# Performance work log

Hardware: AMD Instinct MI355X
Metric: run time of the kernel (lower is better)

Reference implementation:

```python
import jax, jax.numpy as jnp
import numpy as np

B, M, D, H = 2, 2048, 1024, 16
DH = D // H            # 64 head dim
FF = 2624              # GeGLU intermediate size
EPS = 1e-5
ROPE_BASE = 10000.0


def _layernorm(x, g, b):
    mu = jnp.mean(x, axis=-1, keepdims=True)
    var = jnp.mean(jnp.square(x - mu), axis=-1, keepdims=True)
    return (x - mu) * jax.lax.rsqrt(var + EPS) * g + b


def _rope_cos_sin(m, dh):
    # HF-style: inv_freq over even dims; only first dh/2 entries are used by apply_rope
    inv_freq = 1.0 / (ROPE_BASE ** (jnp.arange(0, dh, 2, dtype=jnp.float32) / dh))  # [dh/2]
    ang = jnp.arange(m, dtype=jnp.float32)[:, None] * inv_freq[None, :]             # [M, dh/2]
    return jnp.cos(ang), jnp.sin(ang)


def _apply_rope(x, c, s):
    # x: [B,H,M,dh]; c,s: [M,dh/2] broadcast over B,H. Half-split (non-interleaved) rotation.
    x1, x2 = jnp.split(x, 2, axis=-1)
    return jnp.concatenate([x1 * c - x2 * s, x1 * s + x2 * c], axis=-1)


def setup_inputs() -> dict:
    key = jax.random.key(0)
    ks = jax.random.split(key, 6)
    w = lambda k, shape: (jax.random.normal(k, shape, jnp.float32) * 0.02)
    return {
        "hidden_states": jax.random.normal(ks[0], (B, M, D), jnp.float32),
        "attention_mask": jnp.ones((B, M), jnp.int32),
        "ln1_g": jnp.ones((D,), jnp.float32),
        "ln1_b": jnp.zeros((D,), jnp.float32),
        "Wqkv_w": w(ks[1], (3 * D, D)),
        "Wqkv_b": jnp.zeros((3 * D,), jnp.float32),
        "Wo_w": w(ks[2], (D, D)),
        "ln2_g": jnp.ones((D,), jnp.float32),
        "ln2_b": jnp.zeros((D,), jnp.float32),
        "Wi_w": w(ks[3], (2 * FF, D)),
        "Wmlp_o_w": w(ks[4], (D, FF)),
    }


def reference(hidden_states, attention_mask, ln1_g, ln1_b, Wqkv_w, Wqkv_b, Wo_w,
              ln2_g, ln2_b, Wi_w, Wmlp_o_w):
    x = hidden_states                                    # [B,M,D]
    xn = _layernorm(x, ln1_g, ln1_b)
    qkv = xn @ Wqkv_w.T + Wqkv_b                         # [B,M,3D]
    qkv = qkv.reshape(B, M, 3, H, DH).transpose(0, 3, 1, 2, 4)  # [B,H,M,3,dh]
    q, k, v = qkv[..., 0, :], qkv[..., 1, :], qkv[..., 2, :]    # each [B,H,M,dh]

    c, s = _rope_cos_sin(M, DH)                          # [M, dh/2]
    q = _apply_rope(q, c, s)
    k = _apply_rope(k, c, s)

    scale = 1.0 / np.sqrt(DH)
    scores = jnp.einsum("bhmd,bhnd->bhmn", q, k) * scale  # [B,H,M,M]
    keep = (attention_mask > 0)[:, None, None, :]         # [B,1,1,M] padding mask on keys
    scores = jnp.where(keep, scores, -jnp.inf)
    p = jax.nn.softmax(scores, axis=-1)
    o = jnp.einsum("bhmn,bhnd->bhmd", p, v)               # [B,H,M,dh]

    attn_out = o.transpose(0, 2, 1, 3).reshape(B, M, D)
    x = x + attn_out @ Wo_w.T

    # ModernBERT GeGLU MLP: input, gate = Wi(x).chunk(2); Wo(gelu(input) * gate)
    xn2 = _layernorm(x, ln2_g, ln2_b)
    hg = xn2 @ Wi_w.T                                     # [B,M,2*FF]
    h_in, h_gate = jnp.split(hg, 2, axis=-1)
    x = x + (jax.nn.gelu(h_in) * h_gate) @ Wmlp_o_w.T
    return x
```

## Files before the change

### kernel.cpp

```cpp
#include <hip/hip_runtime.h>
#include <cstdint>
#include <cstddef>

using u16 = unsigned short;
using u32 = uint32_t;

typedef __attribute__((ext_vector_type(8))) short short8;
typedef __attribute__((ext_vector_type(4))) float floatx4;

#define DEVFN static __device__ __forceinline__

#define QSCALE 0.18033688011112042f

DEVFN u16 f2bf(float f) {
  u32 u = __float_as_uint(f);
  return (u16)((u + 0x7fffu + ((u >> 16) & 1u)) >> 16);
}

DEVFN float b2f(u16 u) { return __uint_as_float(((u32)u) << 16); }

DEVFN void async_load16(const void* g, const void* lds) {
  __builtin_amdgcn_global_load_lds(
      (const __attribute__((address_space(1))) u32*)(uintptr_t)g,
      (__attribute__((address_space(3))) u32*)(u32)(uintptr_t)lds,
      16, 0, 0);
}

DEVFN void cvt4(const float* __restrict__ src, u16* __restrict__ dst, int i) {
  const float4 v = ((const float4*)src)[i];
  ushort4 o;
  o.x = f2bf(v.x); o.y = f2bf(v.y); o.z = f2bf(v.z); o.w = f2bf(v.w);
  ((ushort4*)dst)[i] = o;
}

__global__ __launch_bounds__(256)
void prep_k(const float* __restrict__ Wqkv, const float* __restrict__ Wo,
            const float* __restrict__ Wi, const float* __restrict__ Wmlp,
            const float* __restrict__ hidden, const float* __restrict__ ln1g,
            const float* __restrict__ ln1b,
            u16* __restrict__ wqkv_bf, u16* __restrict__ wo_bf,
            u16* __restrict__ wi_bf, u16* __restrict__ wmlp_bf,
            float* __restrict__ ct, float* __restrict__ st, u16* __restrict__ xn) {
  const int bid = blockIdx.x;
  const int tid = threadIdx.x;
  __shared__ float red[8];
  if (bid < 256) {
    const int i = bid * 256 + tid;
    const int m = i >> 5, f = i & 31;
    const float inv = exp2f((float)f * -0.41524101186092025f);
    const float ang = (float)m * inv;
    ct[i] = cosf(ang);
    st[i] = sinf(ang);
  } else if (bid < 3328) {
    cvt4(Wqkv, wqkv_bf, (bid - 256) * 256 + tid);
  } else if (bid < 4352) {
    cvt4(Wo, wo_bf, (bid - 3328) * 256 + tid);
  } else if (bid < 9600) {
    const int i = (bid - 4352) * 256 + tid;
    const int i4 = i * 4;
    const int p = i4 >> 10, kc = i4 & 1023;
    const int g = p >> 5, c = p & 31;
    const int srow = (c < 16) ? (g * 16 + c) : (2624 + g * 16 + (c - 16));
    const float4 v = *(const float4*)(Wi + (size_t)srow * 1024 + kc);
    ushort4 o;
    o.x = f2bf(v.x); o.y = f2bf(v.y); o.z = f2bf(v.z); o.w = f2bf(v.w);
    ((ushort4*)wi_bf)[i] = o;
  } else if (bid < 12224) {
    cvt4(Wmlp, wmlp_bf, (bid - 9600) * 256 + tid);
  } else {
    const int row = bid - 12224;
    const float4 v = ((const float4*)(hidden + (size_t)row * 1024))[tid];
    float s = v.x + v.y + v.z + v.w;
    float ss = v.x * v.x + v.y * v.y + v.z * v.z + v.w * v.w;
#pragma unroll
    for (int d = 32; d > 0; d >>= 1) {
      s += __shfl_xor(s, d);
      ss += __shfl_xor(ss, d);
    }
    const int wave = tid >> 6;
    if ((tid & 63) == 0) { red[wave] = s; red[4 + wave] = ss; }
    __syncthreads();
    s = red[0] + red[1] + red[2] + red[3];
    ss = red[4] + red[5] + red[6] + red[7];
    const float mu = s * (1.f / 1024.f);
    const float var = ss * (1.f / 1024.f) - mu * mu;
    const float rr = rsqrtf(var + 1e-5f);
    const float4 gv = ((const float4*)ln1g)[tid];
    const float4 bv = ((const float4*)ln1b)[tid];
    u16* orow = xn + (size_t)row * 1024 + tid * 4;
    orow[0] = f2bf((v.x - mu) * rr * gv.x + bv.x);
    orow[1] = f2bf((v.y - mu) * rr * gv.y + bv.y);
    orow[2] = f2bf((v.z - mu) * rr * gv.z + bv.z);
    orow[3] = f2bf((v.w - mu) * rr * gv.w + bv.w);
  }
}

__global__ __launch_bounds__(256)
void red_ln_k(const float* __restrict__ resid, const u16* __restrict__ p0,
              const u16* __restrict__ p1, const u16* __restrict__ p2,
              const float* __restrict__ g, const float* __restrict__ bb,
              float* __restrict__ outx, u16* __restrict__ outn) {
  const int row = blockIdx.x;
  const int tid = threadIdx.x;
  const size_t base = (size_t)row * 1024;
  const float4 h = ((const float4*)(resid + base))[tid];
  const ushort4 a = ((const ushort4*)(p0 + base))[tid];
  const ushort4 c = ((const ushort4*)(p1 + base))[tid];
  const ushort4 d = ((const ushort4*)(p2 + base))[tid];
  float4 v;
  v.x = h.x + b2f(a.x) + b2f(c.x) + b2f(d.x);
  v.y = h.y + b2f(a.y) + b2f(c.y) + b2f(d.y);
  v.z = h.z + b2f(a.z) + b2f(c.z) + b2f(d.z);
  v.w = h.w + b2f(a.w) + b2f(c.w) + b2f(d.w);
  float s = v.x + v.y + v.z + v.w;
  float ss = v.x * v.x + v.y * v.y + v.z * v.z + v.w * v.w;
#pragma unroll
  for (int dd = 32; dd > 0; dd >>= 1) {
    s += __shfl_xor(s, dd);
    ss += __shfl_xor(ss, dd);
  }
  __shared__ float red[8];
  const int wave = tid >> 6;
  if ((tid & 63) == 0) { red[wave] = s; red[4 + wave] = ss; }
  __syncthreads();
  s = red[0] + red[1] + red[2] + red[3];
  ss = red[4] + red[5] + red[6] + red[7];
  const float mu = s * (1.f / 1024.f);
  const float var = ss * (1.f / 1024.f) - mu * mu;
  const float rr = rsqrtf(var + 1e-5f);
  ((float4*)(outx + base))[tid] = v;
  const float4 gv = ((const float4*)g)[tid];
  const float4 bv = ((const float4*)bb)[tid];
  u16* orow = outn + base + tid * 4;
  orow[0] = f2bf((v.x - mu) * rr * gv.x + bv.x);
  orow[1] = f2bf((v.y - mu) * rr * gv.y + bv.y);
  orow[2] = f2bf((v.z - mu) * rr * gv.z + bv.z);
  orow[3] = f2bf((v.w - mu) * rr * gv.w + bv.w);
}

__global__ void red_add_k(float* __restrict__ out, const u16* __restrict__ p0,
                          const u16* __restrict__ p1, const u16* __restrict__ p2,
                          const u16* __restrict__ p3) {
  const int i = blockIdx.x * 256 + threadIdx.x;
  float4 v = ((const float4*)out)[i];
  const ushort4 a = ((const ushort4*)p0)[i];
  const ushort4 c = ((const ushort4*)p1)[i];
  const ushort4 d = ((const ushort4*)p2)[i];
  const ushort4 e = ((const ushort4*)p3)[i];
  v.x += b2f(a.x) + b2f(c.x) + b2f(d.x) + b2f(e.x);
  v.y += b2f(a.y) + b2f(c.y) + b2f(d.y) + b2f(e.y);
  v.z += b2f(a.z) + b2f(c.z) + b2f(d.z) + b2f(e.z);
  v.w += b2f(a.w) + b2f(c.w) + b2f(d.w) + b2f(e.w);
  ((float4*)out)[i] = v;
}

DEVFN void swizzle_tile(int NT, int& tn, int& tm) {
  const int tpx = gridDim.x >> 3;
  const int p = blockIdx.x;
  const int lid = (p & 7) * tpx + (p >> 3);
  const int band = lid / (8 * NT);
  const int rem = lid - band * 8 * NT;
  tn = (rem >> 3) * 128;
  tm = (band * 8 + (rem & 7)) * 128;
}

struct EpiArgs {
  const float* bias;
  u16* q; u16* kk; u16* vt;
  u16* outbf;
  const float* ct; const float* st;
};

template <int EPI>
__global__ __launch_bounds__(256, 3)
void gemm_k(const u16* __restrict__ A, const u16* __restrict__ B, int K, int NT,
            EpiArgs ea) {
  __shared__ __align__(16) u16 sA[128 * 32];
  __shared__ __align__(16) u16 sB[128 * 32];
  int tn, tm;
  swizzle_tile(NT, tn, tm);
  const int tid = threadIdx.x;
  const int wave = tid >> 6, lane = tid & 63;
  const int quad = lane >> 4, l15 = lane & 15;
  const int wm = (wave >> 1) * 64, wn = (wave & 1) * 64;

  floatx4 acc[4][4];
#pragma unroll
  for (int i = 0; i < 4; ++i)
#pragma unroll
    for (int j = 0; j < 4; ++j) acc[i][j] = (floatx4){0.f, 0.f, 0.f, 0.f};

  const int srow = lane >> 2;
  const int skc = (lane & 3) * 8;
  const u16* sAr = sA + (wm + l15) * 32 + quad * 8;
  const u16* sBr = sB + (wn + l15) * 32 + quad * 8;

  for (int k0 = 0; k0 < K; k0 += 32) {
#pragma unroll
    for (int j = 0; j < 2; ++j) {
      const int q = wave * 2 + j;
      const int row = q * 16 + srow;
      async_load16(A + (size_t)(tm + row) * K + (k0 + skc), (const char*)sA + q * 1024);
      async_load16(B + (size_t)(tn + row) * K + (k0 + skc), (const char*)sB + q * 1024);
    }
    __syncthreads();
    short8 af[4], bfr[4];
#pragma unroll
    for (int t = 0; t < 4; ++t) af[t] = *(const short8*)(sAr + t * 512);
#pragma unroll
    for (int t = 0; t < 4; ++t) bfr[t] = *(const short8*)(sBr + t * 512);
#pragma unroll
    for (int ti = 0; ti < 4; ++ti)
#pragma unroll
      for (int tj = 0; tj < 4; ++tj)
        acc[ti][tj] = __builtin_amdgcn_mfma_f32_16x16x32_bf16(af[ti], bfr[tj], acc[ti][tj], 0, 0, 0);
    __syncthreads();
  }

  if constexpr (EPI == 0) {
    const int col0 = tn + wn;
    const int t = col0 >> 10;
    const int h = (col0 & 1023) >> 6;
    if (t == 2) {
#pragma unroll
      for (int ti = 0; ti < 4; ++ti)
#pragma unroll
        for (int r = 0; r < 4; ++r) {
          const int row = tm + wm + ti * 16 + quad * 4 + r;
          const int b = row >> 11, m = row & 2047;
          const int mp = (m & ~31) | ((m & 15) << 1) | ((m >> 4) & 1);
#pragma unroll
          for (int tj = 0; tj < 4; ++tj) {
            const int dh = tj * 16 + l15;
            const float v = acc[ti][tj][r] + ea.bias[col0 + dh];
            ea.vt[((size_t)((b * 16 + h) * 64 + dh)) * 2048 + mp] = f2bf(v);
          }
        }
    } else {
      u16* dst = (t == 0) ? ea.q : ea.kk;
      const float qs = (t == 0) ? QSCALE : 1.f;
#pragma unroll
      for (int ti = 0; ti < 4; ++ti)
#pragma unroll
        for (int r = 0; r < 4; ++r) {
          const int row = tm + wm + ti * 16 + quad * 4 + r;
          const int b = row >> 11, m = row & 2047;
          u16* drow = dst + ((size_t)(b * 16 + h) * 2048 + m) * 64;
#pragma unroll
          for (int tj = 0; tj < 2; ++tj) {
            const int i = tj * 16 + l15;
            const float x1 = acc[ti][tj][r] + ea.bias[col0 + i];
            const float x2 = acc[ti][tj + 2][r] + ea.bias[col0 + 32 + i];
            const float cs = ea.ct[m * 32 + i];
            const float sn = ea.st[m * 32 + i];
            drow[i] = f2bf((x1 * cs - x2 * sn) * qs);
            drow[32 + i] = f2bf((x1 * sn + x2 * cs) * qs);
          }
        }
    }
  } else {
#pragma unroll
    for (int ti = 0; ti < 4; ++ti)
#pragma unroll
      for (int r = 0; r < 4; ++r) {
        const int row = tm + wm + ti * 16 + quad * 4 + r;
#pragma unroll
        for (int u = 0; u < 2; ++u) {
          const float hin = acc[ti][2 * u][r];
          const float hg = acc[ti][2 * u + 1][r];
          const int a = (((tn + wn) >> 5) + u) * 16 + l15;
          const float t2 = hin + 0.044715f * hin * hin * hin;
          const float e = __builtin_amdgcn_exp2f(t2 * -2.302114768f);
          const float gl = hin * __builtin_amdgcn_rcpf(1.f + e);
          ea.outbf[(size_t)row * 2624 + a] = f2bf(gl * hg);
        }
      }
  }
}

__global__ __launch_bounds__(256, 3)
void gemm_sk4(const u16* __restrict__ A, const u16* __restrict__ B, int K, int NT,
              int kps1, int zsw, int kps2,
              u16* __restrict__ p0, u16* __restrict__ p1,
              u16* __restrict__ p2, u16* __restrict__ p3) {
  __shared__ __align__(16) u16 sA[128 * 32];
  __shared__ __align__(16) u16 sB[128 * 32];
  int tn, tm;
  swizzle_tile(NT, tn, tm);
  const int z = blockIdx.y;
  int kofs, kps;
  if (z < zsw) { kofs = z * kps1; kps = kps1; }
  else { kofs = zsw * kps1 + (z - zsw) * kps2; kps = kps2; }
  const int tid = threadIdx.x;
  const int wave = tid >> 6, lane = tid & 63;
  const int quad = lane >> 4, l15 = lane & 15;
  const int wm = (wave >> 1) * 64, wn = (wave & 1) * 64;

  floatx4 acc[4][4];
#pragma unroll
  for (int i = 0; i < 4; ++i)
#pragma unroll
    for (int j = 0; j < 4; ++j) acc[i][j] = (floatx4){0.f, 0.f, 0.f, 0.f};

  const int srow = lane >> 2;
  const int skc = (lane & 3) * 8;
  const u16* sAr = sA + (wm + l15) * 32 + quad * 8;
  const u16* sBr = sB + (wn + l15) * 32 + quad * 8;

  for (int k0 = 0; k0 < kps; k0 += 32) {
    const int kk = kofs + k0;
#pragma unroll
    for (int j = 0; j < 2; ++j) {
      const int q = wave * 2 + j;
      const int row = q * 16 + srow;
      async_load16(A + (size_t)(tm + row) * K + (kk + skc), (const char*)sA + q * 1024);
      async_load16(B + (size_t)(tn + row) * K + (kk + skc), (const char*)sB + q * 1024);
    }
    __syncthreads();
    short8 af[4], bfr[4];
#pragma unroll
    for (int t = 0; t < 4; ++t) af[t] = *(const short8*)(sAr + t * 512);
#pragma unroll
    for (int t = 0; t < 4; ++t) bfr[t] = *(const short8*)(sBr + t * 512);
#pragma unroll
    for (int ti = 0; ti < 4; ++ti)
#pragma unroll
      for (int tj = 0; tj < 4; ++tj)
        acc[ti][tj] = __builtin_amdgcn_mfma_f32_16x16x32_bf16(af[ti], bfr[tj], acc[ti][tj], 0, 0, 0);
    __syncthreads();
  }

  u16* part = (z == 0) ? p0 : (z == 1) ? p1 : (z == 2) ? p2 : p3;
#pragma unroll
  for (int ti = 0; ti < 4; ++ti)
#pragma unroll
    for (int r = 0; r < 4; ++r) {
      const int row = tm + wm + ti * 16 + quad * 4 + r;
#pragma unroll
      for (int tj = 0; tj < 4; ++tj)
        part[(size_t)row * 1024 + tn + wn + tj * 16 + l15] = f2bf(acc[ti][tj][r]);
    }
}

__global__ __launch_bounds__(256, 2)
void attn_k(const u16* __restrict__ qg, const u16* __restrict__ kg,
            const u16* __restrict__ vtg, const int* __restrict__ mask,
            u16* __restrict__ outg) {
  __shared__ __align__(16) u16 sK[8 * 128 * 8];
  __shared__ __align__(16) u16 sV[16 * 64 * 8];
  __shared__ __align__(16) u16 sP[8 * 16 * 40];
  const int bh = blockIdx.y;
  const int b = bh >> 4, h = bh & 15;
  const int q0 = blockIdx.x * 128;
  const int tid = threadIdx.x;
  const int wave = tid >> 6, lane = tid & 63;
  const int quad = lane >> 4, l15 = lane & 15;

  short8 aq[2][2];
#pragma unroll
  for (int g = 0; g < 2; ++g) {
    const u16* qptr = qg + ((size_t)bh * 2048 + q0 + wave * 32 + g * 16 + l15) * 64 + quad * 8;
    aq[g][0] = *(const short8*)qptr;
    aq[g][1] = *(const short8*)(qptr + 32);
  }

  floatx4 o[2][4];
#pragma unroll
  for (int g = 0; g < 2; ++g)
#pragma unroll
    for (int t = 0; t < 4; ++t) o[g][t] = (floatx4){0.f, 0.f, 0.f, 0.f};
  float li[2][4] = {{0.f, 0.f, 0.f, 0.f}, {0.f, 0.f, 0.f, 0.f}};

  for (int kt = 0; kt < 16; ++kt) {
    const int key0 = kt * 128;
#pragma unroll
    for (int j = 0; j < 8; ++j) {
      const int qi = wave * 8 + j;
      if (qi < 16) {
        const int chunk = qi >> 1, half = qi & 1;
        const int row = half * 64 + lane;
        async_load16(kg + ((size_t)bh * 2048 + key0 + row) * 64 + chunk * 8,
                     (const char*)sK + qi * 1024);
      } else {
        const int vi = qi - 16;
        const int c = vi >> 2, kc = vi & 3;
        async_load16(vtg + ((size_t)bh * 64 + lane) * 2048 + key0 + c * 32 + kc * 8,
                     (const char*)sV + vi * 1024);
      }
    }
    float mb[8];
#pragma unroll
    for (int tj = 0; tj < 8; ++tj)
      mb[tj] = (mask[b * 2048 + key0 + tj * 16 + l15] > 0) ? 0.f : -1e30f;
    __syncthreads();

    floatx4 sacc[2][8];
#pragma unroll
    for (int g = 0; g < 2; ++g)
#pragma unroll
      for (int tj = 0; tj < 8; ++tj) sacc[g][tj] = (floatx4){0.f, 0.f, 0.f, 0.f};
#pragma unroll
    for (int tj = 0; tj < 8; ++tj) {
      const short8 b0 = *(const short8*)(sK + quad * 1024 + (tj * 16 + l15) * 8);
      const short8 b1 = *(const short8*)(sK + (4 + quad) * 1024 + (tj * 16 + l15) * 8);
      sacc[0][tj] = __builtin_amdgcn_mfma_f32_16x16x32_bf16(aq[0][0], b0, sacc[0][tj], 0, 0, 0);
      sacc[0][tj] = __builtin_amdgcn_mfma_f32_16x16x32_bf16(aq[0][1], b1, sacc[0][tj], 0, 0, 0);
      sacc[1][tj] = __builtin_amdgcn_mfma_f32_16x16x32_bf16(aq[1][0], b0, sacc[1][tj], 0, 0, 0);
      sacc[1][tj] = __builtin_amdgcn_mfma_f32_16x16x32_bf16(aq[1][1], b1, sacc[1][tj], 0, 0, 0);
    }

#pragma unroll
    for (int g = 0; g < 2; ++g)
#pragma unroll
      for (int r = 0; r < 4; ++r) {
        float sum = li[g][r];
#pragma unroll
        for (int tj = 0; tj < 8; ++tj) {
          const float p = __builtin_amdgcn_exp2f(sacc[g][tj][r] + mb[tj]);
          sacc[g][tj][r] = p;
          sum += p;
        }
        li[g][r] = sum;
      }

#pragma unroll
    for (int c = 0; c < 4; ++c) {
#pragma unroll
      for (int g = 0; g < 2; ++g) {
        u32* pw32 = (u32*)sP + (wave * 2 + g) * 320;
#pragma unroll
        for (int r = 0; r < 4; ++r) {
          const u32 lo = __float_as_uint(sacc[g][c * 2][r]) + 0x8000u;
          const u32 hi = __float_as_uint(sacc[g][c * 2 + 1][r]) + 0x8000u;
          pw32[(quad * 4 + r) * 20 + l15] = __builtin_amdgcn_perm(hi, lo, 0x07060302);
        }
      }
      asm volatile("s_waitcnt lgkmcnt(0)" ::: "memory");
      short8 ap[2];
#pragma unroll
      for (int g = 0; g < 2; ++g)
        ap[g] = *(const short8*)(sP + (wave * 2 + g) * 640 + l15 * 40 + quad * 8);
#pragma unroll
      for (int tj2 = 0; tj2 < 4; ++tj2) {
        const short8 bv = *(const short8*)(sV + (c * 4 + quad) * 512 + (tj2 * 16 + l15) * 8);
        o[0][tj2] = __builtin_amdgcn_mfma_f32_16x16x32_bf16(ap[0], bv, o[0][tj2], 0, 0, 0);
        o[1][tj2] = __builtin_amdgcn_mfma_f32_16x16x32_bf16(ap[1], bv, o[1][tj2], 0, 0, 0);
      }
    }
    __syncthreads();
  }

#pragma unroll
  for (int g = 0; g < 2; ++g)
#pragma unroll
    for (int r = 0; r < 4; ++r) {
      float s = li[g][r];
      s += __shfl_xor(s, 1);
      s += __shfl_xor(s, 2);
      s += __shfl_xor(s, 4);
      s += __shfl_xor(s, 8);
      li[g][r] = 1.f / s;
    }

#pragma unroll
  for (int g = 0; g < 2; ++g)
#pragma unroll
    for (int tj = 0; tj < 4; ++tj)
#pragma unroll
      for (int r = 0; r < 4; ++r) {
        const int m = q0 + wave * 32 + g * 16 + quad * 4 + r;
        outg[((size_t)b * 2048 + m) * 1024 + h * 64 + tj * 16 + l15] =
            f2bf(o[g][tj][r] * li[g][r]);
      }
}

static const size_t OFF_WQKV = 0;
static const size_t OFF_WO   = 6291456;
static const size_t OFF_WI   = 8388608;
static const size_t OFF_WMLP = 19136512;
static const size_t OFF_XN   = 24510464;
static const size_t OFF_Q    = 32899072;
static const size_t OFF_K    = 41287680;
static const size_t OFF_VT   = 49676288;
static const size_t OFF_ATT  = 58064896;
static const size_t OFF_ROPE = OFF_ATT;
static const size_t WS_NEED  = 66453504;

extern "C" void kernel_launch(void* const* d_in, const int* in_sizes, int n_in,
                              void* d_out, int out_size, void* d_ws, size_t ws_size,
                              hipStream_t stream) {
  (void)in_sizes; (void)n_in; (void)out_size;
  if (ws_size < WS_NEED) return;

  const float* hidden = (const float*)d_in[0];
  const int*   mask   = (const int*)d_in[1];
  const float* ln1g   = (const float*)d_in[2];
  const float* ln1b   = (const float*)d_in[3];
  const float* Wqkv   = (const float*)d_in[4];
  const float* Wqkvb  = (const float*)d_in[5];
  const float* Wo     = (const float*)d_in[6];
  const float* ln2g   = (const float*)d_in[7];
  const float* ln2b   = (const float*)d_in[8];
  const float* Wi     = (const float*)d_in[9];
  const float* Wmlp   = (const float*)d_in[10];
  float* out = (float*)d_out;
  char* ws = (char*)d_ws;

  u16* wqkv_bf = (u16*)(ws + OFF_WQKV);
  u16* wo_bf   = (u16*)(ws + OFF_WO);
  u16* wi_bf   = (u16*)(ws + OFF_WI);
  u16* wmlp_bf = (u16*)(ws + OFF_WMLP);
  u16* xn      = (u16*)(ws + OFF_XN);
  u16* qb      = (u16*)(ws + OFF_Q);
  u16* kb      = (u16*)(ws + OFF_K);
  u16* vtb     = (u16*)(ws + OFF_VT);
  u16* att     = (u16*)(ws + OFF_ATT);
  u16* act     = (u16*)(ws + OFF_Q);
  float* ct    = (float*)(ws + OFF_ROPE);
  float* st    = (float*)(ws + OFF_ROPE + 262144);
  u16* wp0     = (u16*)(ws + OFF_Q);
  u16* wp1     = (u16*)(ws + OFF_K);
  u16* wp2     = (u16*)(ws + OFF_VT);
  u16* mp0     = (u16*)(ws + OFF_XN);
  u16* mp1     = (u16*)(ws + OFF_ATT);
  u16* mp2     = (u16*)(ws + OFF_WI);
  u16* mp3     = (u16*)(ws + OFF_WQKV);

  prep_k<<<16320, 256, 0, stream>>>(Wqkv, Wo, Wi, Wmlp, hidden, ln1g, ln1b,
                                    wqkv_bf, wo_bf, wi_bf, wmlp_bf, ct, st, xn);

  EpiArgs e1 = {Wqkvb, qb, kb, vtb, nullptr, ct, st};
  gemm_k<0><<<768, 256, 0, stream>>>(xn, wqkv_bf, 1024, 24, e1);

  attn_k<<<dim3(16, 32), 256, 0, stream>>>(qb, kb, vtb, mask, att);

  gemm_sk4<<<dim3(256, 3), 256, 0, stream>>>(att, wo_bf, 1024, 8, 352, 2, 320,
                                             wp0, wp1, wp2, wp2);
  red_ln_k<<<4096, 256, 0, stream>>>(hidden, wp0, wp1, wp2, ln2g, ln2b, out, xn);

  EpiArgs e3 = {nullptr, nullptr, nullptr, nullptr, act, nullptr, nullptr};
  gemm_k<2><<<1312, 256, 0, stream>>>(xn, wi_bf, 1024, 41, e3);

  gemm_sk4<<<dim3(256, 4), 256, 0, stream>>>(act, wmlp_bf, 2624, 8, 672, 2, 640,
                                             mp0, mp1, mp2, mp3);
  red_add_k<<<4096, 256, 0, stream>>>(out, mp0, mp1, mp2, mp3);
}
```

Measured before the change: 349.3 us.

## Double-buffer K/V tiles in attention kernel to overlap loads with compute

Splits the attention K/V shared-memory staging into two buffers. The next tile's async global-to-LDS loads and mask values are issued before computing on the current tile, which removes one barrier per iteration and hides load latency behind the MFMA work. The first MFMA of each score tile now takes a constant zero accumulator, so the explicit zeroing loop is gone. LDS use per block roughly doubles for K/V, which may limit occupancy at two blocks per CU.

```diff
diff --git a/kernel.cpp b/kernel.cpp
--- a/kernel.cpp
+++ b/kernel.cpp
@@ -342,12 +342,31 @@
     }
 }
 
+DEVFN void attn_stage(const u16* __restrict__ kg, const u16* __restrict__ vtg,
+                      size_t bhbase_k, size_t bhbase_v, int key0, int wave,
+                      int lane, const u16* sK, const u16* sV) {
+#pragma unroll
+  for (int j = 0; j < 8; ++j) {
+    const int qi = wave * 8 + j;
+    if (qi < 16) {
+      const int chunk = qi >> 1, half = qi & 1;
+      const int row = half * 64 + lane;
+      async_load16(kg + bhbase_k + (size_t)(key0 + row) * 64 + chunk * 8,
+                   (const char*)sK + qi * 1024);
+    } else {
+      const int vi = qi - 16;
+      const int c = vi >> 2, kc = vi & 3;
+      async_load16(vtg + bhbase_v + (size_t)lane * 2048 + key0 + c * 32 + kc * 8,
+                   (const char*)sV + vi * 1024);
+    }
+  }
+}
+
 __global__ __launch_bounds__(256, 2)
 void attn_k(const u16* __restrict__ qg, const u16* __restrict__ kg,
             const u16* __restrict__ vtg, const int* __restrict__ mask,
             u16* __restrict__ outg) {
-  __shared__ __align__(16) u16 sK[8 * 128 * 8];
-  __shared__ __align__(16) u16 sV[16 * 64 * 8];
+  __shared__ __align__(16) u16 sKV[2][16384];
   __shared__ __align__(16) u16 sP[8 * 16 * 40];
   const int bh = blockIdx.y;
   const int b = bh >> 4, h = bh & 15;
@@ -355,6 +374,8 @@
   const int tid = threadIdx.x;
   const int wave = tid >> 6, lane = tid & 63;
   const int quad = lane >> 4, l15 = lane & 15;
+  const size_t bhk = (size_t)bh * 2048 * 64;
+  const size_t bhv = (size_t)bh * 64 * 2048;
 
   short8 aq[2][2];
 #pragma unroll
@@ -370,42 +391,37 @@
 #pragma unroll
     for (int t = 0; t < 4; ++t) o[g][t] = (floatx4){0.f, 0.f, 0.f, 0.f};
   float li[2][4] = {{0.f, 0.f, 0.f, 0.f}, {0.f, 0.f, 0.f, 0.f}};
-
+  const floatx4 z4 = {0.f, 0.f, 0.f, 0.f};
+
+  float mbc[8];
+#pragma unroll
+  for (int tj = 0; tj < 8; ++tj)
+    mbc[tj] = (mask[b * 2048 + tj * 16 + l15] > 0) ? 0.f : -1e30f;
+
+  attn_stage(kg, vtg, bhk, bhv, 0, wave, lane, sKV[0], sKV[0] + 8192);
+  __syncthreads();
+
+  int buf = 0;
   for (int kt = 0; kt < 16; ++kt) {
-    const int key0 = kt * 128;
-#pragma unroll
-    for (int j = 0; j < 8; ++j) {
-      const int qi = wave * 8 + j;
-      if (qi < 16) {
-        const int chunk = qi >> 1, half = qi & 1;
-        const int row = half * 64 + lane;
-        async_load16(kg + ((size_t)bh * 2048 + key0 + row) * 64 + chunk * 8,
-                     (const char*)sK + qi * 1024);
-      } else {
-        const int vi = qi - 16;
-        const int c = vi >> 2, kc = vi & 3;
-        async_load16(vtg + ((size_t)bh * 64 + lane) * 2048 + key0 + c * 32 + kc * 8,
-                     (const char*)sV + vi * 1024);
-      }
-    }
-    float mb[8];
-#pragma unroll
-    for (int tj = 0; tj < 8; ++tj)
-      mb[tj] = (mask[b * 2048 + key0 + tj * 16 + l15] > 0) ? 0.f : -1e30f;
-    __syncthreads();
+    const u16* sK = sKV[buf];
+    const u16* sV = sKV[buf] + 8192;
+    float mbn[8];
+    if (kt < 15) {
+      attn_stage(kg, vtg, bhk, bhv, (kt + 1) * 128, wave, lane,
+                 sKV[buf ^ 1], sKV[buf ^ 1] + 8192);
+#pragma unroll
+      for (int tj = 0; tj < 8; ++tj)
+        mbn[tj] = (mask[b * 2048 + (kt + 1) * 128 + tj * 16 + l15] > 0) ? 0.f : -1e30f;
+    }
 
     floatx4 sacc[2][8];
-#pragma unroll
-    for (int g = 0; g < 2; ++g)
-#pragma unroll
-      for (int tj = 0; tj < 8; ++tj) sacc[g][tj] = (floatx4){0.f, 0.f, 0.f, 0.f};
 #pragma unroll
     for (int tj = 0; tj < 8; ++tj) {
       const short8 b0 = *(const short8*)(sK + quad * 1024 + (tj * 16 + l15) * 8);
       const short8 b1 = *(const short8*)(sK + (4 + quad) * 1024 + (tj * 16 + l15) * 8);
-      sacc[0][tj] = __builtin_amdgcn_mfma_f32_16x16x32_bf16(aq[0][0], b0, sacc[0][tj], 0, 0, 0);
+      sacc[0][tj] = __builtin_amdgcn_mfma_f32_16x16x32_bf16(aq[0][0], b0, z4, 0, 0, 0);
       sacc[0][tj] = __builtin_amdgcn_mfma_f32_16x16x32_bf16(aq[0][1], b1, sacc[0][tj], 0, 0, 0);
-      sacc[1][tj] = __builtin_amdgcn_mfma_f32_16x16x32_bf16(aq[1][0], b0, sacc[1][tj], 0, 0, 0);
+      sacc[1][tj] = __builtin_amdgcn_mfma_f32_16x16x32_bf16(aq[1][0], b0, z4, 0, 0, 0);
       sacc[1][tj] = __builtin_amdgcn_mfma_f32_16x16x32_bf16(aq[1][1], b1, sacc[1][tj], 0, 0, 0);
     }
 
@@ -416,7 +432,7 @@
         float sum = li[g][r];
 #pragma unroll
         for (int tj = 0; tj < 8; ++tj) {
-          const float p = __builtin_amdgcn_exp2f(sacc[g][tj][r] + mb[tj]);
+          const float p = __builtin_amdgcn_exp2f(sacc[g][tj][r] + mbc[tj]);
           sacc[g][tj][r] = p;
           sum += p;
         }
@@ -448,6 +464,9 @@
       }
     }
     __syncthreads();
+#pragma unroll
+    for (int tj = 0; tj < 8; ++tj) mbc[tj] = mbn[tj];
+    buf ^= 1;
   }
 
 #pragma unroll
```

New measurement: 348.3 us. Within noise of the previous version (-0.3%).

## Double GEMM K-step to 64 with chunk-major LDS layout

Applied to the files above, without the earlier changes.

The GEMM and split-K GEMM kernels now stage a 64-wide K slice per iteration instead of 32, halving the number of barrier pairs per tile. Shared memory is laid out chunk-major ([k-chunk][row][8]) and each wave issues 8 async 16-byte loads, with a whole wave covering 64 consecutive rows of one chunk. The split-K partition sizes are changed to multiples of 64 so every split stays valid. This doubles LDS per block (which may limit occupancy) and changes the split-K balance, including making the last MLP split smaller.

```diff
diff --git a/kernel.cpp b/kernel.cpp
--- a/kernel.cpp
+++ b/kernel.cpp
@@ -164,6 +164,24 @@
   tm = (band * 8 + (rem & 7)) * 128;
 }
 
+DEVFN void gemm_stage64(const u16* __restrict__ A, const u16* __restrict__ B,
+                        int K, int tm, int tn, int k0, int wave, int lane,
+                        const u16* sA, const u16* sB) {
+#pragma unroll
+  for (int j = 0; j < 8; ++j) {
+    const int qi = wave * 8 + j;
+    const int li = qi & 15;
+    const int chunk = li >> 1, half = li & 1;
+    const int row = half * 64 + lane;
+    if (qi < 16)
+      async_load16(A + (size_t)(tm + row) * K + k0 + chunk * 8,
+                   (const char*)sA + li * 1024);
+    else
+      async_load16(B + (size_t)(tn + row) * K + k0 + chunk * 8,
+                   (const char*)sB + li * 1024);
+  }
+}
+
 struct EpiArgs {
   const float* bias;
   u16* q; u16* kk; u16* vt;
@@ -175,8 +193,8 @@
 __global__ __launch_bounds__(256, 3)
 void gemm_k(const u16* __restrict__ A, const u16* __restrict__ B, int K, int NT,
             EpiArgs ea) {
-  __shared__ __align__(16) u16 sA[128 * 32];
-  __shared__ __align__(16) u16 sB[128 * 32];
+  __shared__ __align__(16) u16 sA[8 * 128 * 8];
+  __shared__ __align__(16) u16 sB[8 * 128 * 8];
   int tn, tm;
   swizzle_tile(NT, tn, tm);
   const int tid = threadIdx.x;
@@ -190,30 +208,24 @@
 #pragma unroll
     for (int j = 0; j < 4; ++j) acc[i][j] = (floatx4){0.f, 0.f, 0.f, 0.f};
 
-  const int srow = lane >> 2;
-  const int skc = (lane & 3) * 8;
-  const u16* sAr = sA + (wm + l15) * 32 + quad * 8;
-  const u16* sBr = sB + (wn + l15) * 32 + quad * 8;
-
-  for (int k0 = 0; k0 < K; k0 += 32) {
-#pragma unroll
-    for (int j = 0; j < 2; ++j) {
-      const int q = wave * 2 + j;
-      const int row = q * 16 + srow;
-      async_load16(A + (size_t)(tm + row) * K + (k0 + skc), (const char*)sA + q * 1024);
-      async_load16(B + (size_t)(tn + row) * K + (k0 + skc), (const char*)sB + q * 1024);
-    }
-    __syncthreads();
-    short8 af[4], bfr[4];
-#pragma unroll
-    for (int t = 0; t < 4; ++t) af[t] = *(const short8*)(sAr + t * 512);
-#pragma unroll
-    for (int t = 0; t < 4; ++t) bfr[t] = *(const short8*)(sBr + t * 512);
-#pragma unroll
-    for (int ti = 0; ti < 4; ++ti)
-#pragma unroll
-      for (int tj = 0; tj < 4; ++tj)
-        acc[ti][tj] = __builtin_amdgcn_mfma_f32_16x16x32_bf16(af[ti], bfr[tj], acc[ti][tj], 0, 0, 0);
+  for (int k0 = 0; k0 < K; k0 += 64) {
+    gemm_stage64(A, B, K, tm, tn, k0, wave, lane, sA, sB);
+    __syncthreads();
+#pragma unroll
+    for (int s = 0; s < 2; ++s) {
+      short8 af[4], bfr[4];
+#pragma unroll
+      for (int t = 0; t < 4; ++t)
+        af[t] = *(const short8*)(sA + (((s * 4 + quad) * 128) + wm + t * 16 + l15) * 8);
+#pragma unroll
+      for (int t = 0; t < 4; ++t)
+        bfr[t] = *(const short8*)(sB + (((s * 4 + quad) * 128) + wn + t * 16 + l15) * 8);
+#pragma unroll
+      for (int ti = 0; ti < 4; ++ti)
+#pragma unroll
+        for (int tj = 0; tj < 4; ++tj)
+          acc[ti][tj] = __builtin_amdgcn_mfma_f32_16x16x32_bf16(af[ti], bfr[tj], acc[ti][tj], 0, 0, 0);
+    }
     __syncthreads();
   }
 
@@ -283,8 +295,8 @@
               int kps1, int zsw, int kps2,
               u16* __restrict__ p0, u16* __restrict__ p1,
               u16* __restrict__ p2, u16* __restrict__ p3) {
-  __shared__ __align__(16) u16 sA[128 * 32];
-  __shared__ __align__(16) u16 sB[128 * 32];
+  __shared__ __align__(16) u16 sA[8 * 128 * 8];
+  __shared__ __align__(16) u16 sB[8 * 128 * 8];
   int tn, tm;
   swizzle_tile(NT, tn, tm);
   const int z = blockIdx.y;
@@ -302,31 +314,24 @@
 #pragma unroll
     for (int j = 0; j < 4; ++j) acc[i][j] = (floatx4){0.f, 0.f, 0.f, 0.f};
 
-  const int srow = lane >> 2;
-  const int skc = (lane & 3) * 8;
-  const u16* sAr = sA + (wm + l15) * 32 + quad * 8;
-  const u16* sBr = sB + (wn + l15) * 32 + quad * 8;
-
-  for (int k0 = 0; k0 < kps; k0 += 32) {
-    const int kk = kofs + k0;
-#pragma unroll
-    for (int j = 0; j < 2; ++j) {
-      const int q = wave * 2 + j;
-      const int row = q * 16 + srow;
-      async_load16(A + (size_t)(tm + row) * K + (kk + skc), (const char*)sA + q * 1024);
-      async_load16(B + (size_t)(tn + row) * K + (kk + skc), (const char*)sB + q * 1024);
-    }
-    __syncthreads();
-    short8 af[4], bfr[4];
-#pragma unroll
-    for (int t = 0; t < 4; ++t) af[t] = *(const short8*)(sAr + t * 512);
-#pragma unroll
-    for (int t = 0; t < 4; ++t) bfr[t] = *(const short8*)(sBr + t * 512);
-#pragma unroll
-    for (int ti = 0; ti < 4; ++ti)
-#pragma unroll
-      for (int tj = 0; tj < 4; ++tj)
-        acc[ti][tj] = __builtin_amdgcn_mfma_f32_16x16x32_bf16(af[ti], bfr[tj], acc[ti][tj], 0, 0, 0);
+  for (int k0 = 0; k0 < kps; k0 += 64) {
+    gemm_stage64(A, B, K, tm, tn, kofs + k0, wave, lane, sA, sB);
+    __syncthreads();
+#pragma unroll
+    for (int s = 0; s < 2; ++s) {
+      short8 af[4], bfr[4];
+#pragma unroll
+      for (int t = 0; t < 4; ++t)
+        af[t] = *(const short8*)(sA + (((s * 4 + quad) * 128) + wm + t * 16 + l15) * 8);
+#pragma unroll
+      for (int t = 0; t < 4; ++t)
+        bfr[t] = *(const short8*)(sB + (((s * 4 + quad) * 128) + wn + t * 16 + l15) * 8);
+#pragma unroll
+      for (int ti = 0; ti < 4; ++ti)
+#pragma unroll
+        for (int tj = 0; tj < 4; ++tj)
+          acc[ti][tj] = __builtin_amdgcn_mfma_f32_16x16x32_bf16(af[ti], bfr[tj], acc[ti][tj], 0, 0, 0);
+    }
     __syncthreads();
   }
 
@@ -534,14 +539,14 @@
 
   attn_k<<<dim3(16, 32), 256, 0, stream>>>(qb, kb, vtb, mask, att);
 
-  gemm_sk4<<<dim3(256, 3), 256, 0, stream>>>(att, wo_bf, 1024, 8, 352, 2, 320,
+  gemm_sk4<<<dim3(256, 3), 256, 0, stream>>>(att, wo_bf, 1024, 8, 384, 2, 256,
                                              wp0, wp1, wp2, wp2);
   red_ln_k<<<4096, 256, 0, stream>>>(hidden, wp0, wp1, wp2, ln2g, ln2b, out, xn);
 
   EpiArgs e3 = {nullptr, nullptr, nullptr, nullptr, act, nullptr, nullptr};
   gemm_k<2><<<1312, 256, 0, stream>>>(xn, wi_bf, 1024, 41, e3);
 
-  gemm_sk4<<<dim3(256, 4), 256, 0, stream>>>(act, wmlp_bf, 2624, 8, 672, 2, 640,
+  gemm_sk4<<<dim3(256, 4), 256, 0, stream>>>(act, wmlp_bf, 2624, 8, 704, 1, 640,
                                              mp0, mp1, mp2, mp3);
   red_add_k<<<4096, 256, 0, stream>>>(out, mp0, mp1, mp2, mp3);
 }
```

Result: slower. 455.2 us (+30.3%).
